# Optimization experiments

Measured on AMD Instinct MI355X. Metric: run time of the kernel, lower is better.

The kernel has to match this reference:

```python
import jax, jax.numpy as jnp
import numpy as np


def _greedy_match(d):
    # d: [S, S] pairwise distances. Greedy bipartite match: repeatedly take
    # global argmin, record pred_row -> gt_col, mask out that row and column.
    S = d.shape[0]

    def body(i, carry):
        dm, matches = carry
        m = jnp.argmin(dm.reshape(-1))
        r = m // S
        c = m % S
        matches = matches.at[r].set(c)
        dm = dm.at[r, :].set(jnp.inf)
        dm = dm.at[:, c].set(jnp.inf)
        return dm, matches

    _, matches = jax.lax.fori_loop(0, S, body, (d, jnp.zeros((S,), jnp.int32)))
    return matches


def setup_inputs() -> dict:
    key = jax.random.key(0)
    k1, k2 = jax.random.split(key)
    bs, seq_len, n_sources, input_dim = 8, 4096, 4, 257
    predictions = jax.random.normal(k1, (bs, seq_len, n_sources, input_dim), jnp.float32)
    ground_truths = jax.random.normal(k2, (bs, seq_len, n_sources, input_dim), jnp.float32)
    return {"predictions": predictions, "ground_truths": ground_truths}


def reference(predictions, ground_truths):
    # predictions, ground_truths: [bs, seq_len, S, D]
    bs, seq_len, S, D = predictions.shape
    # Flatten each source's full time-frequency signal: [bs, S, seq_len*D]
    p = jnp.transpose(predictions, (0, 2, 1, 3)).reshape(bs, S, seq_len * D)
    g = jnp.transpose(ground_truths, (0, 2, 1, 3)).reshape(bs, S, seq_len * D)

    # Euclidean cdist between pred sources and gt sources: [bs, S, S]
    d2 = (jnp.sum(p * p, axis=-1)[:, :, None]
          + jnp.sum(g * g, axis=-1)[:, None, :]
          - 2.0 * jnp.einsum('bsk,btk->bst', p, g))
    dists = jnp.sqrt(jnp.maximum(d2, 0.0))

    # Greedy assignment (ranks are monotone in distance, so matching on the
    # distances directly is identical to matching on the argsort-rank matrix).
    matches = jax.vmap(_greedy_match)(jax.lax.stop_gradient(dists))  # [bs, S] int32

    # Per-(batch, pred-source) distance to its matched gt source:
    # torch.norm(pred[b] - gt_match[b]) == euclidean dist of flattened vectors.
    gm = jnp.take_along_axis(g, matches[:, :, None], axis=1)  # [bs, S, seq_len*D]
    per = jnp.linalg.norm(p - gm, axis=-1)  # [bs, S]

    return jnp.sum(per) / bs
```

## Files before the change

kernel.cpp:

```cpp
#include <hip/hip_runtime.h>
#include <math.h>

#define BS 8
#define T  4096
#define D  257
#define SD 1028
#define ROWS 2
#define TILE_FLOATS (ROWS * SD)
#define BPB 128
#define NT  16
#define NACC 24
#define NBLK (BS * BPB)

__global__ __launch_bounds__(256) void zero_ws_kernel(float* ws) {
    int i = blockIdx.x * blockDim.x + threadIdx.x;
    if (i < BS * NACC) ws[i] = 0.0f;
}

__device__ __forceinline__ void gload16(const float* g, float* l) {
    __builtin_amdgcn_global_load_lds(
        (const __attribute__((address_space(1))) unsigned int*)g,
        (__attribute__((address_space(3))) unsigned int*)l,
        16, 0, 0);
}

template <int DIRECT>
__global__ __launch_bounds__(256) void partial_kernel(const float* __restrict__ P,
                                                      const float* __restrict__ G,
                                                      float* __restrict__ ws) {
    __shared__ float ldsP[2][TILE_FLOATS];
    __shared__ float ldsG[2][TILE_FLOATS];
    __shared__ float sm[4][NACC];

    const int tid  = threadIdx.x;
    const int lane = tid & 63;
    const int wv   = tid >> 6;
    const int b    = blockIdx.x >> 7;
    const int blkb = blockIdx.x & (BPB - 1);

    const float* __restrict__ Pb = P + (size_t)b * T * SD;
    const float* __restrict__ Gb = G + (size_t)b * T * SD;

    float acc[NACC];
    #pragma unroll
    for (int k = 0; k < NACC; ++k) acc[k] = 0.0f;

    auto stage = [&](int buf, int it) {
        const int rg = blkb + it * BPB;
        const float* srcP = Pb + (size_t)rg * TILE_FLOATS;
        const float* srcG = Gb + (size_t)rg * TILE_FLOATS;
        #pragma unroll
        for (int c = 0; c < 2; ++c) {
            const int off = (wv * 2 + c) * 256;
            gload16(srcP + off + lane * 4, &ldsP[buf][off]);
            gload16(srcG + off + lane * 4, &ldsG[buf][off]);
        }
        if (wv == 0 && lane < 2) gload16(srcP + 2048 + lane * 4, &ldsP[buf][2048]);
        if (wv == 1 && lane < 2) gload16(srcG + 2048 + lane * 4, &ldsG[buf][2048]);
    };

    auto process = [&](int cur, int base) {
        const float p0 = ldsP[cur][base];
        const float p1 = ldsP[cur][base + D];
        const float p2 = ldsP[cur][base + 2 * D];
        const float p3 = ldsP[cur][base + 3 * D];
        const float g0 = ldsG[cur][base];
        const float g1 = ldsG[cur][base + D];
        const float g2 = ldsG[cur][base + 2 * D];
        const float g3 = ldsG[cur][base + 3 * D];
        acc[0] = fmaf(p0, p0, acc[0]);  acc[1] = fmaf(p1, p1, acc[1]);
        acc[2] = fmaf(p2, p2, acc[2]);  acc[3] = fmaf(p3, p3, acc[3]);
        acc[4] = fmaf(g0, g0, acc[4]);  acc[5] = fmaf(g1, g1, acc[5]);
        acc[6] = fmaf(g2, g2, acc[6]);  acc[7] = fmaf(g3, g3, acc[7]);
        acc[ 8] = fmaf(p0, g0, acc[ 8]); acc[ 9] = fmaf(p0, g1, acc[ 9]);
        acc[10] = fmaf(p0, g2, acc[10]); acc[11] = fmaf(p0, g3, acc[11]);
        acc[12] = fmaf(p1, g0, acc[12]); acc[13] = fmaf(p1, g1, acc[13]);
        acc[14] = fmaf(p1, g2, acc[14]); acc[15] = fmaf(p1, g3, acc[15]);
        acc[16] = fmaf(p2, g0, acc[16]); acc[17] = fmaf(p2, g1, acc[17]);
        acc[18] = fmaf(p2, g2, acc[18]); acc[19] = fmaf(p2, g3, acc[19]);
        acc[20] = fmaf(p3, g0, acc[20]); acc[21] = fmaf(p3, g1, acc[21]);
        acc[22] = fmaf(p3, g2, acc[22]); acc[23] = fmaf(p3, g3, acc[23]);
    };

    stage(0, 0);
    for (int it = 0; it < NT; ++it) {
        const int cur = it & 1;
        if (it + 1 < NT) {
            stage(cur ^ 1, it + 1);
            if (wv < 2) asm volatile("s_waitcnt vmcnt(5)" ::: "memory");
            else        asm volatile("s_waitcnt vmcnt(4)" ::: "memory");
        } else {
            asm volatile("s_waitcnt vmcnt(0)" ::: "memory");
        }
        __builtin_amdgcn_s_barrier();
        __builtin_amdgcn_sched_barrier(0);

        process(cur, tid);
        process(cur, SD + tid);
        if (tid < 2) process(cur, tid * SD + 256);

        __builtin_amdgcn_sched_barrier(0);
        __builtin_amdgcn_s_barrier();
    }

    #pragma unroll
    for (int k = 0; k < NACC; ++k) {
        float v = acc[k];
        #pragma unroll
        for (int o = 32; o > 0; o >>= 1) v += __shfl_down(v, o, 64);
        if (lane == 0) sm[wv][k] = v;
    }
    __syncthreads();
    if (tid < NACC) {
        float v = sm[0][tid] + sm[1][tid] + sm[2][tid] + sm[3][tid];
        if (DIRECT) ws[blockIdx.x * NACC + tid] = v;
        else        atomicAdd(&ws[b * NACC + tid], v);
    }
}

__device__ __forceinline__ float greedy_total(const float* w8x24 ) {
    float total = 0.f;
    for (int b = 0; b < BS; ++b) {
        const float* w = w8x24 + b * NACC;
        float dist[16];
        for (int s = 0; s < 4; ++s)
            for (int t = 0; t < 4; ++t) {
                float d2 = w[s] + w[4 + t] - 2.f * w[8 + s * 4 + t];
                dist[s * 4 + t] = sqrtf(fmaxf(d2, 0.f));
            }
        bool rdone[4] = {false, false, false, false};
        bool cdone[4] = {false, false, false, false};
        for (int it = 0; it < 4; ++it) {
            float best = INFINITY; int br = 0, bc = 0;
            bool found = false;
            for (int s = 0; s < 4; ++s) {
                if (rdone[s]) continue;
                for (int t = 0; t < 4; ++t) {
                    if (cdone[t]) continue;
                    float v = dist[s * 4 + t];
                    if (!found || v < best) { best = v; br = s; bc = t; found = true; }
                }
            }
            total += best;
            rdone[br] = true; cdone[bc] = true;
        }
    }
    return total * 0.125f;
}

__global__ __launch_bounds__(256) void finalize_direct_kernel(const float* __restrict__ ws,
                                                              float* __restrict__ out) {
    __shared__ float wsm[BS * NACC];
    const int t = threadIdx.x;
    if (t < BS * NACC) {
        const int b = t / NACC, k = t - b * NACC;
        float v = 0.f;
        for (int j = 0; j < BPB; ++j)
            v += ws[((size_t)(b * BPB + j)) * NACC + k];
        wsm[t] = v;
    }
    __syncthreads();
    if (t == 0) *out = greedy_total(wsm);
}

__global__ void finalize_atomic_kernel(const float* __restrict__ ws, float* __restrict__ out) {
    if (threadIdx.x != 0 || blockIdx.x != 0) return;
    *out = greedy_total(ws);
}

extern "C" void kernel_launch(void* const* d_in, const int* in_sizes, int n_in,
                              void* d_out, int out_size, void* d_ws, size_t ws_size,
                              hipStream_t stream) {
    const float* P = (const float*)d_in[0];
    const float* G = (const float*)d_in[1];
    float* out = (float*)d_out;
    float* ws  = (float*)d_ws;

    if (ws_size >= (size_t)NBLK * NACC * sizeof(float)) {
        partial_kernel<1><<<NBLK, 256, 0, stream>>>(P, G, ws);
        finalize_direct_kernel<<<1, 256, 0, stream>>>(ws, out);
    } else {
        zero_ws_kernel<<<1, 256, 0, stream>>>(ws);
        partial_kernel<0><<<NBLK, 256, 0, stream>>>(P, G, ws);
        finalize_atomic_kernel<<<1, 64, 0, stream>>>(ws, out);
    }
}
```

Baseline: 75.66 us.

## Replace LDS-staged tiles with direct strided loads and a nontemporal tail

Removes the async global-to-LDS double-buffered pipeline and barriers. Each thread now reads P and G straight from global memory with a grid-stride loop over the flattened (t,d) positions. Block count rises to 256 per batch, and the block order is interleaved across batches. The first 14 strides use normal cached loads and the remainder use nontemporal loads, apparently so a hot portion stays resident in cache across repeated calls. The direct loads fetch single floats per lane at a stride that is not 16-byte aligned, which may cost bandwidth versus the 16-byte LDS loads.

```diff
diff --git a/kernel.cpp b/kernel.cpp
--- a/kernel.cpp
+++ b/kernel.cpp
@@ -5,38 +5,63 @@
 #define T  4096
 #define D  257
 #define SD 1028
-#define ROWS 2
-#define TILE_FLOATS (ROWS * SD)
-#define BPB 128
-#define NT  16
+#define K  (T * D)
 #define NACC 24
+#define BPB 256
 #define NBLK (BS * BPB)
+#define STRIDE (BPB * 256)
+#define KHOT (14 * STRIDE)
 
 __global__ __launch_bounds__(256) void zero_ws_kernel(float* ws) {
     int i = blockIdx.x * blockDim.x + threadIdx.x;
     if (i < BS * NACC) ws[i] = 0.0f;
 }
 
-__device__ __forceinline__ void gload16(const float* g, float* l) {
-    __builtin_amdgcn_global_load_lds(
-        (const __attribute__((address_space(1))) unsigned int*)g,
-        (__attribute__((address_space(3))) unsigned int*)l,
-        16, 0, 0);
+template <int NT>
+__device__ __forceinline__ void process_pos(const float* __restrict__ Pb,
+                                            const float* __restrict__ Gb,
+                                            int i, float* acc) {
+    const int t = i / D;
+    const int d = i - t * D;
+    const float* p = Pb + (size_t)t * SD + d;
+    const float* g = Gb + (size_t)t * SD + d;
+    float p0, p1, p2, p3, g0, g1, g2, g3;
+    if (NT) {
+        p0 = __builtin_nontemporal_load(p);
+        p1 = __builtin_nontemporal_load(p + D);
+        p2 = __builtin_nontemporal_load(p + 2 * D);
+        p3 = __builtin_nontemporal_load(p + 3 * D);
+        g0 = __builtin_nontemporal_load(g);
+        g1 = __builtin_nontemporal_load(g + D);
+        g2 = __builtin_nontemporal_load(g + 2 * D);
+        g3 = __builtin_nontemporal_load(g + 3 * D);
+    } else {
+        p0 = p[0]; p1 = p[D]; p2 = p[2 * D]; p3 = p[3 * D];
+        g0 = g[0]; g1 = g[D]; g2 = g[2 * D]; g3 = g[3 * D];
+    }
+    acc[0] = fmaf(p0, p0, acc[0]);  acc[1] = fmaf(p1, p1, acc[1]);
+    acc[2] = fmaf(p2, p2, acc[2]);  acc[3] = fmaf(p3, p3, acc[3]);
+    acc[4] = fmaf(g0, g0, acc[4]);  acc[5] = fmaf(g1, g1, acc[5]);
+    acc[6] = fmaf(g2, g2, acc[6]);  acc[7] = fmaf(g3, g3, acc[7]);
+    acc[ 8] = fmaf(p0, g0, acc[ 8]); acc[ 9] = fmaf(p0, g1, acc[ 9]);
+    acc[10] = fmaf(p0, g2, acc[10]); acc[11] = fmaf(p0, g3, acc[11]);
+    acc[12] = fmaf(p1, g0, acc[12]); acc[13] = fmaf(p1, g1, acc[13]);
+    acc[14] = fmaf(p1, g2, acc[14]); acc[15] = fmaf(p1, g3, acc[15]);
+    acc[16] = fmaf(p2, g0, acc[16]); acc[17] = fmaf(p2, g1, acc[17]);
+    acc[18] = fmaf(p2, g2, acc[18]); acc[19] = fmaf(p2, g3, acc[19]);
+    acc[20] = fmaf(p3, g0, acc[20]); acc[21] = fmaf(p3, g1, acc[21]);
+    acc[22] = fmaf(p3, g2, acc[22]); acc[23] = fmaf(p3, g3, acc[23]);
 }
 
 template <int DIRECT>
 __global__ __launch_bounds__(256) void partial_kernel(const float* __restrict__ P,
                                                       const float* __restrict__ G,
                                                       float* __restrict__ ws) {
-    __shared__ float ldsP[2][TILE_FLOATS];
-    __shared__ float ldsG[2][TILE_FLOATS];
-    __shared__ float sm[4][NACC];
-
     const int tid  = threadIdx.x;
     const int lane = tid & 63;
     const int wv   = tid >> 6;
-    const int b    = blockIdx.x >> 7;
-    const int blkb = blockIdx.x & (BPB - 1);
+    const int b    = blockIdx.x & 7;
+    const int blkb = blockIdx.x >> 3;
 
     const float* __restrict__ Pb = P + (size_t)b * T * SD;
     const float* __restrict__ Gb = G + (size_t)b * T * SD;
@@ -45,64 +70,13 @@
     #pragma unroll
     for (int k = 0; k < NACC; ++k) acc[k] = 0.0f;
 
-    auto stage = [&](int buf, int it) {
-        const int rg = blkb + it * BPB;
-        const float* srcP = Pb + (size_t)rg * TILE_FLOATS;
-        const float* srcG = Gb + (size_t)rg * TILE_FLOATS;
-        #pragma unroll
-        for (int c = 0; c < 2; ++c) {
-            const int off = (wv * 2 + c) * 256;
-            gload16(srcP + off + lane * 4, &ldsP[buf][off]);
-            gload16(srcG + off + lane * 4, &ldsG[buf][off]);
-        }
-        if (wv == 0 && lane < 2) gload16(srcP + 2048 + lane * 4, &ldsP[buf][2048]);
-        if (wv == 1 && lane < 2) gload16(srcG + 2048 + lane * 4, &ldsG[buf][2048]);
-    };
+    int i = blkb * 256 + tid;
+    for (; i < KHOT; i += STRIDE)
+        process_pos<0>(Pb, Gb, i, acc);
+    for (; i < K; i += STRIDE)
+        process_pos<1>(Pb, Gb, i, acc);
 
-    auto process = [&](int cur, int base) {
-        const float p0 = ldsP[cur][base];
-        const float p1 = ldsP[cur][base + D];
-        const float p2 = ldsP[cur][base + 2 * D];
-        const float p3 = ldsP[cur][base + 3 * D];
-        const float g0 = ldsG[cur][base];
-        const float g1 = ldsG[cur][base + D];
-        const float g2 = ldsG[cur][base + 2 * D];
-        const float g3 = ldsG[cur][base + 3 * D];
-        acc[0] = fmaf(p0, p0, acc[0]);  acc[1] = fmaf(p1, p1, acc[1]);
-        acc[2] = fmaf(p2, p2, acc[2]);  acc[3] = fmaf(p3, p3, acc[3]);
-        acc[4] = fmaf(g0, g0, acc[4]);  acc[5] = fmaf(g1, g1, acc[5]);
-        acc[6] = fmaf(g2, g2, acc[6]);  acc[7] = fmaf(g3, g3, acc[7]);
-        acc[ 8] = fmaf(p0, g0, acc[ 8]); acc[ 9] = fmaf(p0, g1, acc[ 9]);
-        acc[10] = fmaf(p0, g2, acc[10]); acc[11] = fmaf(p0, g3, acc[11]);
-        acc[12] = fmaf(p1, g0, acc[12]); acc[13] = fmaf(p1, g1, acc[13]);
-        acc[14] = fmaf(p1, g2, acc[14]); acc[15] = fmaf(p1, g3, acc[15]);
-        acc[16] = fmaf(p2, g0, acc[16]); acc[17] = fmaf(p2, g1, acc[17]);
-        acc[18] = fmaf(p2, g2, acc[18]); acc[19] = fmaf(p2, g3, acc[19]);
-        acc[20] = fmaf(p3, g0, acc[20]); acc[21] = fmaf(p3, g1, acc[21]);
-        acc[22] = fmaf(p3, g2, acc[22]); acc[23] = fmaf(p3, g3, acc[23]);
-    };
-
-    stage(0, 0);
-    for (int it = 0; it < NT; ++it) {
-        const int cur = it & 1;
-        if (it + 1 < NT) {
-            stage(cur ^ 1, it + 1);
-            if (wv < 2) asm volatile("s_waitcnt vmcnt(5)" ::: "memory");
-            else        asm volatile("s_waitcnt vmcnt(4)" ::: "memory");
-        } else {
-            asm volatile("s_waitcnt vmcnt(0)" ::: "memory");
-        }
-        __builtin_amdgcn_s_barrier();
-        __builtin_amdgcn_sched_barrier(0);
-
-        process(cur, tid);
-        process(cur, SD + tid);
-        if (tid < 2) process(cur, tid * SD + 256);
-
-        __builtin_amdgcn_sched_barrier(0);
-        __builtin_amdgcn_s_barrier();
-    }
-
+    __shared__ float sm[4][NACC];
     #pragma unroll
     for (int k = 0; k < NACC; ++k) {
         float v = acc[k];
@@ -156,7 +130,7 @@
         const int b = t / NACC, k = t - b * NACC;
         float v = 0.f;
         for (int j = 0; j < BPB; ++j)
-            v += ws[((size_t)(b * BPB + j)) * NACC + k];
+            v += ws[((size_t)j * 8 + b) * NACC + k];
         wsm[t] = v;
     }
     __syncthreads();
```

Result: no change. 75.14 us (-0.7%).
